# Optimization experiments

Measured on AMD Instinct MI355X. Metric: run time of the kernel, lower is better.

## Reference

```python
import jax, jax.numpy as jnp
import numpy as np

B, H0, W0, D0 = 2, 28, 28, 28
C, NH, SR, WS = 96, 6, 4, 7
N = H0 * W0 * D0
EPS = 1e-5


def _window_partition(x, ws, H, W, D):
    # x: [B, heads, N, c] -> [B*heads*nWindows, ws^3, c]
    Bn, h, Nn, c = x.shape
    x = x.reshape(Bn * h, H // ws, ws, W // ws, ws, D // ws, ws, c)
    x = x.transpose(0, 1, 3, 5, 2, 4, 6, 7)
    return x.reshape(-1, ws * ws * ws, c)


def _window_reverse(w, ws, H, W, D, heads):
    # w: [B*heads*nWindows, ws^3, c] -> [B, N, heads*c]
    c = w.shape[-1]
    nW = (H // ws) * (W // ws) * (D // ws)
    Bh = w.shape[0] // nW
    x = w.reshape(Bh, H // ws, W // ws, D // ws, ws, ws, ws, c)
    x = x.transpose(0, 1, 4, 2, 5, 3, 6, 7).reshape(Bh, H, W, D, c)
    x = x.reshape(Bh // heads, heads, H, W, D, c).transpose(0, 2, 3, 4, 1, 5)
    return x.reshape(Bh // heads, H * W * D, heads * c)


def _ln(x, g, b):
    mu = x.mean(-1, keepdims=True)
    var = ((x - mu) ** 2).mean(-1, keepdims=True)
    return (x - mu) * jax.lax.rsqrt(var + EPS) * g + b


def _forward(x, H, W, D, lepe_lin_w, lepe_lin_b, lepe_conv_w, lepe_conv_b,
             sr_w, sr_b, norm_g, norm_b, q1_w, kv1_w, q2_w, kv2_w, proj_w, proj_b):
    Bn, Nn, Cc = x.shape
    nh2 = NH // 2
    hd = Cc // NH
    scale = hd ** -0.5
    dn = ('NCDHW', 'OIDHW', 'NCDHW')
    # LePE branch: linear -> depthwise 3x3x3 conv over the 3D volume
    t = (x @ lepe_lin_w.T + lepe_lin_b).transpose(0, 2, 1).reshape(Bn, Cc, H, W, D)
    lepe = jax.lax.conv_general_dilated(t, lepe_conv_w, (1, 1, 1), [(1, 1)] * 3,
                                        dimension_numbers=dn, feature_group_count=Cc)
    lepe = (lepe + lepe_conv_b[None, :, None, None, None]).reshape(Bn, Cc, Nn).transpose(0, 2, 1)
    # Branch 1: spatial-reduction global attention on half the heads
    q1 = (x @ q1_w.T).reshape(Bn, Nn, nh2, hd).transpose(0, 2, 1, 3)  # [B,h/2,N,hd]
    x5 = x.transpose(0, 2, 1).reshape(Bn, Cc, H, W, D)
    xs = jax.lax.conv_general_dilated(x5, sr_w, (SR, SR, SR), 'VALID', dimension_numbers=dn)
    xs = (xs + sr_b[None, :, None, None, None]).reshape(Bn, Cc, -1).transpose(0, 2, 1)  # [B,Nsr,C]
    xs = jax.nn.gelu(_ln(xs, norm_g, norm_b), approximate=False)
    kv1 = (xs @ kv1_w.T).reshape(Bn, -1, 2, nh2, hd).transpose(2, 0, 3, 1, 4)
    k1, v1 = kv1[0], kv1[1]
    attn1 = jax.nn.softmax(jnp.einsum('bhnd,bhmd->bhnm', q1, k1) * scale, axis=-1)
    x1 = jnp.einsum('bhnm,bhmd->bhnd', attn1, v1).transpose(0, 2, 1, 3).reshape(Bn, Nn, Cc // 2)
    # Branch 2: 7x7x7 windowed local attention on the other half of the heads
    q2 = (x @ q2_w.T).reshape(Bn, Nn, nh2, hd).transpose(0, 2, 1, 3)
    kv2 = (x @ kv2_w.T).reshape(Bn, Nn, 2, nh2, hd).transpose(2, 0, 3, 1, 4)
    k2, v2 = kv2[0], kv2[1]
    q2w = _window_partition(q2, WS, H, W, D)
    k2w = _window_partition(k2, WS, H, W, D)
    v2w = _window_partition(v2, WS, H, W, D)
    attn2 = jax.nn.softmax(jnp.einsum('wnd,wmd->wnm', q2w, k2w) * scale, axis=-1)
    x2 = _window_reverse(jnp.einsum('wnm,wmd->wnd', attn2, v2w), WS, H, W, D, nh2)
    # Fuse branches, add LePE, project
    return (jnp.concatenate([x1, x2], axis=-1) + lepe) @ proj_w.T + proj_b


def setup_inputs() -> dict:
    key = jax.random.key(0)
    ks = jax.random.split(key, 10)
    lin = lambda k, o, i: jax.random.normal(k, (o, i), jnp.float32) * 0.02
    return {
        'x': jax.random.normal(ks[0], (B, N, C), jnp.float32),
        'H': H0, 'W': W0, 'D': D0,
        'lepe_lin_w': lin(ks[1], C, C),
        'lepe_lin_b': jnp.zeros((C,), jnp.float32),
        'lepe_conv_w': jax.random.normal(ks[2], (C, 1, 3, 3, 3), jnp.float32) * 0.27,
        'lepe_conv_b': jnp.zeros((C,), jnp.float32),
        'sr_w': jax.random.normal(ks[3], (C, C, SR, SR, SR), jnp.float32) * 0.02,
        'sr_b': jnp.zeros((C,), jnp.float32),
        'norm_g': jnp.ones((C,), jnp.float32),
        'norm_b': jnp.zeros((C,), jnp.float32),
        'q1_w': lin(ks[4], C // 2, C),
        'kv1_w': lin(ks[5], C, C),
        'q2_w': lin(ks[6], C // 2, C),
        'kv2_w': lin(ks[7], C, C),
        'proj_w': lin(ks[8], C, C),
        'proj_b': jnp.zeros((C,), jnp.float32),
    }


def reference(x, H, W, D, lepe_lin_w, lepe_lin_b, lepe_conv_w, lepe_conv_b,
              sr_w, sr_b, norm_g, norm_b, q1_w, kv1_w, q2_w, kv2_w, proj_w, proj_b):
    return _forward(x, H, W, D, lepe_lin_w, lepe_lin_b, lepe_conv_w, lepe_conv_b,
                    sr_w, sr_b, norm_g, norm_b, q1_w, kv1_w, q2_w, kv2_w, proj_w, proj_b)
```

## Files before the change

kernel.cpp:

```cpp
#include <hip/hip_runtime.h>

#define BB 2
#define NTOK 21952
#define CC 96
#define WD 784
#define NSR 343
#define NKT 22
#define NPADK 9.f
#define NSITE 686
#define SCALE 0.25f
#define LN_EPS 1e-5f
#define LNB 4116
#define WSA_N (6*16*24*64)
#define WPA_N (18*6*64)

typedef _Float16 half_t;
typedef __attribute__((ext_vector_type(2))) _Float16 h2;
typedef __attribute__((ext_vector_type(4))) _Float16 h4;
typedef __attribute__((ext_vector_type(8))) _Float16 h8;
typedef __attribute__((ext_vector_type(4))) float f32x4;
union HU { h8 v; h2 p[4]; };
union H4U { h4 v; h2 p[2]; };

__device__ __forceinline__ h2 pk2(float a, float b) {
    return __builtin_bit_cast(h2, __builtin_amdgcn_cvt_pkrtz(a, b));
}

__global__ __launch_bounds__(256) void k_wt(
    const float* __restrict__ w, h4* __restrict__ WSA, h4* __restrict__ WPA,
    const float* __restrict__ lepe_w, const float* __restrict__ q1_w,
    const float* __restrict__ q2_w, const float* __restrict__ kv2_w,
    const float* __restrict__ cw, float* __restrict__ cwT)
{
    const int id = blockIdx.x * 256 + threadIdx.x;
    if (id < WSA_N) {
        const int lane = id & 63;
        const int kt = (id >> 6) % 24;
        const int ks = ((id >> 6) / 24) % 16;
        const int ct = (id >> 6) / 384;
        const int co = ct * 16 + (lane & 15);
        const int kb = ks * 384 + kt * 16 + 4 * (lane >> 4);
        const int p = kb / 96, c = kb % 96;
        float f[4];
#pragma unroll
        for (int i = 0; i < 4; i++)
            f[i] = w[(size_t)co * 6144 + (c + i) * 64 + p];
        H4U t; t.p[0] = pk2(f[0], f[1]); t.p[1] = pk2(f[2], f[3]);
        WSA[id] = t.v;
    } else if (id < WSA_N + WPA_N) {
        const int id2 = id - WSA_N;
        const int lane = id2 & 63;
        const int kt = (id2 >> 6) % 6;
        const int ct = (id2 >> 6) / 6;
        const int co = ct * 16 + (lane & 15);
        const int k = kt * 16 + 4 * (lane >> 4);
        const float* wrow;
        if (co < 96)       wrow = lepe_w + co * 96;
        else if (co < 144) wrow = q1_w + (co - 96) * 96;
        else if (co < 192) wrow = q2_w + (co - 144) * 96;
        else               wrow = kv2_w + (co - 192) * 96;
        float4 v = *(const float4*)(wrow + k);
        H4U t; t.p[0] = pk2(v.x, v.y); t.p[1] = pk2(v.z, v.w);
        WPA[id2] = t.v;
    } else if (id < WSA_N + WPA_N + 27 * 96) {
        const int id3 = id - WSA_N - WPA_N;
        const int tap = id3 / 96, c = id3 % 96;
        cwT[tap * 96 + c] = cw[c * 27 + tap];
    }
}

__global__ __launch_bounds__(256) void k_proj(
    const float* __restrict__ x, const h4* __restrict__ WPA,
    const float* __restrict__ lepe_b, float* __restrict__ P)
{
    __shared__ h4 BX[4 * 6 * 64];
    const int blk = blockIdx.x;
    const int tid = threadIdx.x;

    for (int s = tid; s < 1536; s += 256) {
        int lane = s & 63;
        int kt = (s >> 6) % 6;
        int tt = (s >> 6) / 6;
        int tok = blk * 64 + tt * 16 + (lane & 15);
        int k0 = kt * 16 + 4 * (lane >> 4);
        float4 v = *(const float4*)(x + (size_t)tok * 96 + k0);
        H4U t; t.p[0] = pk2(v.x, v.y); t.p[1] = pk2(v.z, v.w);
        BX[s] = t.v;
    }
    __syncthreads();

    const int lane = tid & 63;
    const int wid = tid >> 6;

    h4 bx[24];
#pragma unroll
    for (int q = 0; q < 24; q++) bx[q] = BX[q * 64 + lane];

    for (int ct = wid; ct < 18; ct += 4) {
        f32x4 acc[4];
#pragma unroll
        for (int tt = 0; tt < 4; tt++) acc[tt] = (f32x4){0.f, 0.f, 0.f, 0.f};
#pragma unroll
        for (int kt = 0; kt < 6; kt++) {
            h4 wa = WPA[(ct * 6 + kt) * 64 + lane];
#pragma unroll
            for (int tt = 0; tt < 4; tt++)
                acc[tt] = __builtin_amdgcn_mfma_f32_16x16x16f16(
                    wa, bx[tt * 6 + kt], acc[tt], 0, 0, 0);
        }
        float4 b4 = make_float4(0.f, 0.f, 0.f, 0.f);
        if (ct < 6) b4 = *(const float4*)(lepe_b + ct * 16 + 4 * (lane >> 4));
#pragma unroll
        for (int tt = 0; tt < 4; tt++) {
            int tok = blk * 64 + tt * 16 + (lane & 15);
            float4 o = make_float4(acc[tt][0] + b4.x, acc[tt][1] + b4.y,
                                   acc[tt][2] + b4.z, acc[tt][3] + b4.w);
            *(float4*)(P + (size_t)tok * 288 + ct * 16 + 4 * (lane >> 4)) = o;
        }
    }
}

__global__ __launch_bounds__(384) void k_sr_a(
    const float* __restrict__ x, const h4* __restrict__ WSA,
    float* __restrict__ pa)
{
    __shared__ h4 BX[24 * 64];
    const int mb = blockIdx.x;
    const int ks = blockIdx.y;
    const int tid = threadIdx.x;
    const int lane = tid & 63;
    const int ct = tid >> 6;

    for (int s = tid; s < 24 * 64; s += 384) {
        int l = s & 63;
        int kt = s >> 6;
        int site = mb * 16 + (l & 15);
        if (site > NSITE - 1) site = NSITE - 1;
        int b = site / NSR, sloc = site % NSR;
        int si = sloc / 49, sj = (sloc / 7) % 7, sk = sloc % 7;
        int kg = ks * 384 + kt * 16 + 4 * (l >> 4);
        int p = kg / 96, c = kg % 96;
        int a = p >> 4, q = (p >> 2) & 3, r = p & 3;
        int n = (4 * si + a) * WD + (4 * sj + q) * 28 + (4 * sk + r);
        float4 v = *(const float4*)(x + ((size_t)b * NTOK + n) * 96 + c);
        H4U t; t.p[0] = pk2(v.x, v.y); t.p[1] = pk2(v.z, v.w);
        BX[s] = t.v;
    }
    __syncthreads();

    const int site_g = mb * 16 + (lane & 15);
    const h4* wb = WSA + (size_t)((ct * 16 + ks) * 24) * 64 + lane;

    f32x4 acc0 = (f32x4){0.f, 0.f, 0.f, 0.f};
    f32x4 acc1 = (f32x4){0.f, 0.f, 0.f, 0.f};
#pragma unroll
    for (int kp = 0; kp < 12; kp++) {
        h4 wa0 = wb[(2 * kp) * 64];
        h4 wa1 = wb[(2 * kp + 1) * 64];
        acc0 = __builtin_amdgcn_mfma_f32_16x16x16f16(
            wa0, BX[(2 * kp) * 64 + lane], acc0, 0, 0, 0);
        acc1 = __builtin_amdgcn_mfma_f32_16x16x16f16(
            wa1, BX[(2 * kp + 1) * 64 + lane], acc1, 0, 0, 0);
    }
    if (site_g < NSITE) {
        *(float4*)(pa + ((size_t)site_g * 16 + ks) * 96 + ct * 16
                   + 4 * (lane >> 4)) =
            make_float4(acc0[0] + acc1[0], acc0[1] + acc1[1],
                        acc0[2] + acc1[2], acc0[3] + acc1[3]);
    }
}

__global__ __launch_bounds__(96) void k_sr_b(
    const float* __restrict__ pa, const float* __restrict__ sr_b,
    const float* __restrict__ norm_g, const float* __restrict__ norm_b,
    const float* __restrict__ kv1_w, float* __restrict__ k1,
    float* __restrict__ v1)
{
    __shared__ float xs_s[96];
    __shared__ float gx[96];
    const int s_g = blockIdx.x;
    const int b = s_g / NSR, s = s_g % NSR;
    const int co = threadIdx.x;

    const float* pp = pa + (size_t)s_g * 16 * 96 + co;
    float acc = sr_b[co];
#pragma unroll
    for (int ks = 0; ks < 16; ks++) acc += pp[ks * 96];
    xs_s[co] = acc;
    __syncthreads();

    float m = 0.f, m2 = 0.f;
    for (int c = 0; c < 96; c++) { float v = xs_s[c]; m += v; m2 += v * v; }
    m *= (1.f / 96.f);
    float var = m2 * (1.f / 96.f) - m * m;
    float t = (acc - m) * rsqrtf(var + LN_EPS) * norm_g[co] + norm_b[co];
    gx[co] = 0.5f * t * (1.f + erff(t * 0.70710678118654752f));
    __syncthreads();

    const float4* w4 = (const float4*)(kv1_w + co * 96);
    const float4* g4 = (const float4*)gx;
    float a2 = 0.f;
#pragma unroll
    for (int c = 0; c < 24; c++) {
        float4 w = w4[c]; float4 g = g4[c];
        a2 += g.x * w.x + g.y * w.y + g.z * w.z + g.w * w.w;
    }
    int pair = co / 48, h = (co % 48) / 16, e = co % 16;
    float* dst = pair ? v1 : k1;
    dst[(((size_t)b * 3 + h) * NSR + s) * 16 + e] = a2;
}

__device__ __forceinline__ void attn_mfma_core(
    const h4* __restrict__ KA, const h4* __restrict__ VA, int lane,
    h4 qb, f32x4& o, float& lsum)
{
    o = (f32x4){0.f, 0.f, 0.f, 0.f};
    lsum = 0.f;
    for (int t = 0; t < NKT; t++) {
        h4 ka = KA[t * 64 + lane];
        f32x4 s = __builtin_amdgcn_mfma_f32_16x16x16f16(
            ka, qb, (f32x4){0.f, 0.f, 0.f, 0.f}, 0, 0, 0);
        float p0 = __expf(s[0]), p1 = __expf(s[1]);
        float p2 = __expf(s[2]), p3 = __expf(s[3]);
        lsum += (p0 + p1) + (p2 + p3);
        H4U pb;
        pb.p[0] = pk2(p0, p1);
        pb.p[1] = pk2(p2, p3);
        h4 va = VA[t * 64 + lane];
        o = __builtin_amdgcn_mfma_f32_16x16x16f16(va, pb.v, o, 0, 0, 0);
    }
}

__global__ __launch_bounds__(512) void k_attn1(
    const float* __restrict__ P, const float* __restrict__ k1,
    const float* __restrict__ v1, float* __restrict__ y)
{
    __shared__ h4 KA[NKT * 64];
    __shared__ h4 VA[NKT * 64];
    const int bh = blockIdx.x;
    const int b = bh / 3, h = bh % 3;
    const float* ksrc = k1 + (size_t)bh * NSR * 16;
    const float* vsrc = v1 + (size_t)bh * NSR * 16;

    for (int s = threadIdx.x; s < NKT * 64; s += 512) {
        int t = s >> 6, l = s & 63;
        int key = t * 16 + (l & 15);
        int dg = (l >> 4) * 4;
        H4U tmp; tmp.p[0] = pk2(0.f, 0.f); tmp.p[1] = pk2(0.f, 0.f);
        if (key < NSR) {
            float4 v = *(const float4*)(ksrc + (size_t)key * 16 + dg);
            tmp.p[0] = pk2(v.x, v.y); tmp.p[1] = pk2(v.z, v.w);
        }
        KA[s] = tmp.v;
    }
    for (int s = threadIdx.x; s < NKT * 64; s += 512) {
        int t = s >> 6, l = s & 63;
        int dim = l & 15;
        int k0 = t * 16 + (l >> 4) * 4;
        float f[4];
#pragma unroll
        for (int i = 0; i < 4; i++) {
            int key = k0 + i;
            f[i] = (key < NSR) ? vsrc[(size_t)key * 16 + dim] : 0.f;
        }
        H4U tmp; tmp.p[0] = pk2(f[0], f[1]); tmp.p[1] = pk2(f[2], f[3]);
        VA[s] = tmp.v;
    }
    __syncthreads();

    const int lane = threadIdx.x & 63;
    const int wid = threadIdx.x >> 6;

    for (int qi = wid; qi < 16; qi += 8) {
        int qt = blockIdx.y * 16 + qi;
        if (qt >= 1372) break;
        int tok = qt * 16 + (lane & 15);
        float4 qv = *(const float4*)(P + ((size_t)b * NTOK + tok) * 288
                                     + 96 + h * 16 + (lane >> 4) * 4);
        H4U qb;
        qb.p[0] = pk2(qv.x * SCALE, qv.y * SCALE);
        qb.p[1] = pk2(qv.z * SCALE, qv.w * SCALE);

        f32x4 o; float lsum;
        attn_mfma_core(KA, VA, lane, qb.v, o, lsum);
        lsum += __shfl_xor(lsum, 16);
        lsum += __shfl_xor(lsum, 32);
        float inv = 1.f / (lsum - NPADK);
        float4 out = make_float4(o[0] * inv, o[1] * inv, o[2] * inv, o[3] * inv);
        *(float4*)(y + ((size_t)b * NTOK + tok) * 96 + h * 16 + (lane >> 4) * 4) = out;
    }
}

__global__ __launch_bounds__(512) void k_attn2(
    const float* __restrict__ P, float* __restrict__ y)
{
    __shared__ h4 KA[NKT * 64];
    __shared__ h4 VA[NKT * 64];
    const int pb = blockIdx.x;
    const int b = pb / 192;
    const int rem = pb % 192;
    const int h = rem / 64, win = rem % 64;
    const int wh = win >> 4, ww = (win >> 2) & 3, wd = win & 3;
    const int h0 = wh * 7, w0 = ww * 7, d0 = wd * 7;
    const size_t bOff = (size_t)b * NTOK;

    for (int s = threadIdx.x; s < NKT * 64; s += 512) {
        int t = s >> 6, l = s & 63;
        int key = t * 16 + (l & 15);
        int dg = (l >> 4) * 4;
        H4U tmp; tmp.p[0] = pk2(0.f, 0.f); tmp.p[1] = pk2(0.f, 0.f);
        if (key < NSR) {
            int a = key / 49, bw = (key / 7) % 7, cw = key % 7;
            int n = (h0 + a) * WD + (w0 + bw) * 28 + (d0 + cw);
            float4 v = *(const float4*)(P + (bOff + n) * 288 + 192 + h * 16 + dg);
            tmp.p[0] = pk2(v.x, v.y); tmp.p[1] = pk2(v.z, v.w);
        }
        KA[s] = tmp.v;
    }
    for (int s = threadIdx.x; s < NKT * 64; s += 512) {
        int t = s >> 6, l = s & 63;
        int dim = l & 15;
        int k0 = t * 16 + (l >> 4) * 4;
        float f[4];
#pragma unroll
        for (int i = 0; i < 4; i++) {
            int key = k0 + i;
            float val = 0.f;
            if (key < NSR) {
                int a = key / 49, bw = (key / 7) % 7, cw = key % 7;
                int n = (h0 + a) * WD + (w0 + bw) * 28 + (d0 + cw);
                val = P[(bOff + n) * 288 + 240 + h * 16 + dim];
            }
            f[i] = val;
        }
        H4U tmp; tmp.p[0] = pk2(f[0], f[1]); tmp.p[1] = pk2(f[2], f[3]);
        VA[s] = tmp.v;
    }
    __syncthreads();

    const int lane = threadIdx.x & 63;
    const int wid = threadIdx.x >> 6;

    for (int qt = wid; qt < NKT; qt += 8) {
        int q = qt * 16 + (lane & 15);
        int qc = (q < NSR) ? q : (NSR - 1);
        int ai = qc / 49, bi = (qc / 7) % 7, ci = qc % 7;
        int tok = (h0 + ai) * WD + (w0 + bi) * 28 + (d0 + ci);
        float4 qv = *(const float4*)(P + (bOff + tok) * 288
                                     + 144 + h * 16 + (lane >> 4) * 4);
        H4U qb;
        qb.p[0] = pk2(qv.x * SCALE, qv.y * SCALE);
        qb.p[1] = pk2(qv.z * SCALE, qv.w * SCALE);

        f32x4 o; float lsum;
        attn_mfma_core(KA, VA, lane, qb.v, o, lsum);
        lsum += __shfl_xor(lsum, 16);
        lsum += __shfl_xor(lsum, 32);
        float inv = 1.f / (lsum - NPADK);
        if (q < NSR) {
            float4 out = make_float4(o[0] * inv, o[1] * inv, o[2] * inv, o[3] * inv);
            *(float4*)(y + (bOff + tok) * 96 + 48 + h * 16 + (lane >> 4) * 4) = out;
        }
    }
}

__global__ __launch_bounds__(256) void k_lepe(
    const float* __restrict__ P, const float* __restrict__ cwT,
    const float* __restrict__ cb, float* __restrict__ y)
{
    const int p = blockIdx.x;
    const int l = (p & 7) * 515 + (p >> 3);
    if (l >= LNB) return;
    const int id = l * 256 + threadIdx.x;
    const int g4 = (id % 24) * 4;
    const int nl = id / 24;
    const int n = nl % NTOK;
    const int h = n / WD, w = (n / 28) % 28, d = n % 28;
    const float* Pb = P + (size_t)(nl - n) * 288;

    float4 acc = *(const float4*)(cb + g4);
#pragma unroll
    for (int tap = 0; tap < 27; tap++) {
        const int dh = tap / 9 - 1, dw = (tap / 3) % 3 - 1, dd = tap % 3 - 1;
        const int hh = h + dh, ww = w + dw, d2 = d + dd;
        const bool v = ((unsigned)hh < 28u) & ((unsigned)ww < 28u) & ((unsigned)d2 < 28u);
        const int nn = v ? (hh * WD + ww * 28 + d2) : n;
        const float m = v ? 1.f : 0.f;
        float4 pv = *(const float4*)(Pb + (size_t)nn * 288 + g4);
        float4 wv = *(const float4*)(cwT + tap * 96 + g4);
        acc.x += pv.x * (wv.x * m);
        acc.y += pv.y * (wv.y * m);
        acc.z += pv.z * (wv.z * m);
        acc.w += pv.w * (wv.w * m);
    }
    float4* yp = (float4*)(y + (size_t)nl * 96 + g4);
    float4 cur = *yp;
    cur.x += acc.x; cur.y += acc.y; cur.z += acc.z; cur.w += acc.w;
    *yp = cur;
}

__global__ __launch_bounds__(192) void k_out(
    const float* __restrict__ y, const float* __restrict__ proj_w,
    const float* __restrict__ proj_b, float* __restrict__ out)
{
    __shared__ h2 xh[48][68];
    __shared__ h2 wh[48][52];

    const int base = blockIdx.x * 64;
    const int j0 = blockIdx.y * 48;

    for (int it = threadIdx.x; it < 1536; it += 192) {
        int t = it & 63, cq = it >> 6;
        float4 v = *(const float4*)(y + (size_t)(base + t) * 96 + cq * 4);
        xh[cq * 2 + 0][t] = pk2(v.x, v.y);
        xh[cq * 2 + 1][t] = pk2(v.z, v.w);
    }
    for (int it = threadIdx.x; it < 1152; it += 192) {
        int jl = it % 48, cq = it / 48;
        float4 v = *(const float4*)(proj_w + (size_t)(j0 + jl) * 96 + cq * 4);
        wh[cq * 2 + 0][jl] = pk2(v.x, v.y);
        wh[cq * 2 + 1][jl] = pk2(v.z, v.w);
    }
    __syncthreads();

    const int tq = threadIdx.x & 15;
    const int jq = threadIdx.x >> 4;
    float acc[4][4];
#pragma unroll
    for (int i = 0; i < 4; i++)
#pragma unroll
        for (int jj = 0; jj < 4; jj++) acc[i][jj] = 0.f;

    for (int cp = 0; cp < 48; cp++) {
        HU xv, wv;
        xv.v = *(const h8*)(&xh[cp][tq * 4]);
        wv.v = *(const h8*)(&wh[cp][jq * 4]);
#pragma unroll
        for (int i = 0; i < 4; i++)
#pragma unroll
            for (int jj = 0; jj < 4; jj++)
                acc[i][jj] = __builtin_amdgcn_fdot2(xv.p[i], wv.p[jj], acc[i][jj], false);
    }

    float4 bias = *(const float4*)(proj_b + j0 + jq * 4);
#pragma unroll
    for (int i = 0; i < 4; i++) {
        int t = base + tq * 4 + i;
        float4 o = make_float4(acc[i][0] + bias.x, acc[i][1] + bias.y,
                               acc[i][2] + bias.z, acc[i][3] + bias.w);
        *(float4*)(out + (size_t)t * 96 + j0 + jq * 4) = o;
    }
}

extern "C" void kernel_launch(void* const* d_in, const int* in_sizes, int n_in,
                              void* d_out, int out_size, void* d_ws, size_t ws_size,
                              hipStream_t stream) {
    const float* x          = (const float*)d_in[0];
    const float* lepe_lin_w = (const float*)d_in[4];
    const float* lepe_lin_b = (const float*)d_in[5];
    const float* lepe_conv_w= (const float*)d_in[6];
    const float* lepe_conv_b= (const float*)d_in[7];
    const float* sr_w       = (const float*)d_in[8];
    const float* sr_b       = (const float*)d_in[9];
    const float* norm_g     = (const float*)d_in[10];
    const float* norm_b     = (const float*)d_in[11];
    const float* q1_w       = (const float*)d_in[12];
    const float* kv1_w      = (const float*)d_in[13];
    const float* q2_w       = (const float*)d_in[14];
    const float* kv2_w      = (const float*)d_in[15];
    const float* proj_w     = (const float*)d_in[16];
    const float* proj_b     = (const float*)d_in[17];

    float* P   = (float*)d_ws;
    float* k1  = P + (size_t)BB * NTOK * 288;
    float* v1  = k1 + (size_t)BB * 3 * NSR * 16;
    float* y   = v1 + (size_t)BB * 3 * NSR * 16;
    float* pa  = y + (size_t)BB * NTOK * 96;
    float* WSAf= pa + (size_t)NSITE * 16 * 96;
    float* WPAf= WSAf + (size_t)WSA_N * 2;
    float* cwT = WPAf + (size_t)WPA_N * 2;
    h4* WSA = (h4*)WSAf;
    h4* WPA = (h4*)WPAf;

    k_wt<<<614, 256, 0, stream>>>(sr_w, WSA, WPA, lepe_lin_w, q1_w, q2_w,
                                  kv2_w, lepe_conv_w, cwT);
    k_proj<<<686, 256, 0, stream>>>(x, WPA, lepe_lin_b, P);
    k_sr_a<<<dim3(43, 16), 384, 0, stream>>>(x, WSA, pa);
    k_sr_b<<<NSITE, 96, 0, stream>>>(pa, sr_b, norm_g, norm_b, kv1_w, k1, v1);
    k_attn1<<<dim3(6, 86), 512, 0, stream>>>(P, k1, v1, y);
    k_attn2<<<384, 512, 0, stream>>>(P, y);
    k_lepe<<<4120, 256, 0, stream>>>(P, cwT, lepe_conv_b, y);
    k_out<<<dim3(686, 2), 192, 0, stream>>>(y, proj_w, proj_b, (float*)d_out);
}
```

Baseline: 220.4 us.

## Register-tile LePE depthwise conv along depth to reuse neighbor loads

Each thread in the depthwise 3x3x3 LePE convolution now computes seven consecutive depth positions instead of one. It loads a 9-element depth strip per (dh,dw) pair and reuses it across the seven outputs and three depth taps. This cuts redundant global/L2 loads and index arithmetic. The trade-off is far fewer threads (588 blocks), higher register pressure, and loss of the earlier block-order swizzle.

```diff
diff --git a/kernel.cpp b/kernel.cpp
--- a/kernel.cpp
+++ b/kernel.cpp
@@ -10,7 +10,6 @@
 #define NSITE 686
 #define SCALE 0.25f
 #define LN_EPS 1e-5f
-#define LNB 4116
 #define WSA_N (6*16*24*64)
 #define WPA_N (18*6*64)
 
@@ -368,35 +367,66 @@
     const float* __restrict__ P, const float* __restrict__ cwT,
     const float* __restrict__ cb, float* __restrict__ y)
 {
-    const int p = blockIdx.x;
-    const int l = (p & 7) * 515 + (p >> 3);
-    if (l >= LNB) return;
-    const int id = l * 256 + threadIdx.x;
+    const int id = blockIdx.x * 256 + threadIdx.x;
     const int g4 = (id % 24) * 4;
-    const int nl = id / 24;
-    const int n = nl % NTOK;
-    const int h = n / WD, w = (n / 28) % 28, d = n % 28;
-    const float* Pb = P + (size_t)(nl - n) * 288;
-
-    float4 acc = *(const float4*)(cb + g4);
-#pragma unroll
-    for (int tap = 0; tap < 27; tap++) {
-        const int dh = tap / 9 - 1, dw = (tap / 3) % 3 - 1, dd = tap % 3 - 1;
-        const int hh = h + dh, ww = w + dw, d2 = d + dd;
-        const bool v = ((unsigned)hh < 28u) & ((unsigned)ww < 28u) & ((unsigned)d2 < 28u);
-        const int nn = v ? (hh * WD + ww * 28 + d2) : n;
-        const float m = v ? 1.f : 0.f;
-        float4 pv = *(const float4*)(Pb + (size_t)nn * 288 + g4);
-        float4 wv = *(const float4*)(cwT + tap * 96 + g4);
-        acc.x += pv.x * (wv.x * m);
-        acc.y += pv.y * (wv.y * m);
-        acc.z += pv.z * (wv.z * m);
-        acc.w += pv.w * (wv.w * m);
-    }
-    float4* yp = (float4*)(y + (size_t)nl * 96 + g4);
-    float4 cur = *yp;
-    cur.x += acc.x; cur.y += acc.y; cur.z += acc.z; cur.w += acc.w;
-    *yp = cur;
+    const int rest = id / 24;
+    const int dc = rest % 4;
+    const int nw = rest / 4;
+    const int w = nw % 28;
+    const int h = (nw / 28) % 28;
+    const int b = nw / 784;
+    const int d0 = dc * 7;
+    const float* Pb = P + (size_t)b * NTOK * 288;
+
+    float4 bias = *(const float4*)(cb + g4);
+    float4 acc[7];
+#pragma unroll
+    for (int j = 0; j < 7; j++) acc[j] = bias;
+
+#pragma unroll
+    for (int dh = -1; dh <= 1; dh++) {
+#pragma unroll
+        for (int dw = -1; dw <= 1; dw++) {
+            const int hh = h + dh, ww = w + dw;
+            const bool pok = ((unsigned)hh < 28u) & ((unsigned)ww < 28u);
+            const int nbase = (pok ? hh : h) * WD + (pok ? ww : w) * 28;
+            const float mp = pok ? 1.f : 0.f;
+            const int tb = ((dh + 1) * 3 + (dw + 1)) * 3;
+            float4 wm = *(const float4*)(cwT + (tb + 0) * 96 + g4);
+            float4 w0 = *(const float4*)(cwT + (tb + 1) * 96 + g4);
+            float4 wp = *(const float4*)(cwT + (tb + 2) * 96 + g4);
+            wm.x *= mp; wm.y *= mp; wm.z *= mp; wm.w *= mp;
+            w0.x *= mp; w0.y *= mp; w0.z *= mp; w0.w *= mp;
+            wp.x *= mp; wp.y *= mp; wp.z *= mp; wp.w *= mp;
+
+            float4 pv[9];
+#pragma unroll
+            for (int k = 0; k < 9; k++) {
+                const int d = d0 + k - 1;
+                const bool dok = (unsigned)d < 28u;
+                float4 v = *(const float4*)(Pb + (size_t)(nbase + (dok ? d : 0)) * 288 + g4);
+                if (!dok) v = make_float4(0.f, 0.f, 0.f, 0.f);
+                pv[k] = v;
+            }
+#pragma unroll
+            for (int j = 0; j < 7; j++) {
+                acc[j].x += pv[j].x * wm.x + pv[j + 1].x * w0.x + pv[j + 2].x * wp.x;
+                acc[j].y += pv[j].y * wm.y + pv[j + 1].y * w0.y + pv[j + 2].y * wp.y;
+                acc[j].z += pv[j].z * wm.z + pv[j + 1].z * w0.z + pv[j + 2].z * wp.z;
+                acc[j].w += pv[j].w * wm.w + pv[j + 1].w * w0.w + pv[j + 2].w * wp.w;
+            }
+        }
+    }
+
+    const size_t tokBase = (size_t)b * NTOK + h * WD + w * 28 + d0;
+#pragma unroll
+    for (int j = 0; j < 7; j++) {
+        float4* yp = (float4*)(y + (tokBase + j) * 96 + g4);
+        float4 cur = *yp;
+        cur.x += acc[j].x; cur.y += acc[j].y;
+        cur.z += acc[j].z; cur.w += acc[j].w;
+        *yp = cur;
+    }
 }
 
 __global__ __launch_bounds__(192) void k_out(
@@ -489,6 +519,6 @@
     k_sr_b<<<NSITE, 96, 0, stream>>>(pa, sr_b, norm_g, norm_b, kv1_w, k1, v1);
     k_attn1<<<dim3(6, 86), 512, 0, stream>>>(P, k1, v1, y);
     k_attn2<<<384, 512, 0, stream>>>(P, y);
-    k_lepe<<<4120, 256, 0, stream>>>(P, cwT, lepe_conv_b, y);
+    k_lepe<<<588, 256, 0, stream>>>(P, cwT, lepe_conv_b, y);
     k_out<<<dim3(686, 2), 192, 0, stream>>>(y, proj_w, proj_b, (float*)d_out);
 }
```

Measured after the change: 218.9 us. No clear change (-0.7%).
